# Optimization experiments

Hardware: AMD Instinct MI355X
Metric: run time of the kernel (lower is better)

The kernel has to match this reference:

```python
import jax, jax.numpy as jnp
import numpy as np

N = 16384   # total nodes
E = 49152   # total edges (avg degree 3, molecular)
NG = 512    # graphs in batch
DIM = 64    # hidden dim
NF = 11     # node features
EF = 4      # edge features
HID = 128   # edge-MLP hidden
JUMPS = 3
S2S_STEPS = 3


def _gru_step(x, h, w_ih, w_hh, b_ih, b_hh):
    gi = x @ w_ih.T + b_ih
    gh = h @ w_hh.T + b_hh
    ir, iz, inn = jnp.split(gi, 3, axis=-1)
    hr, hz, hn = jnp.split(gh, 3, axis=-1)
    r = jax.nn.sigmoid(ir + hr)
    z = jax.nn.sigmoid(iz + hz)
    n = jnp.tanh(inn + r * hn)
    return (1.0 - z) * n + z * h


def _lstm_step(x, h, c, w_ih, w_hh, b_ih, b_hh):
    g = x @ w_ih.T + b_ih + h @ w_hh.T + b_hh
    i, f, gg, o = jnp.split(g, 4, axis=-1)
    c2 = jax.nn.sigmoid(f) * c + jax.nn.sigmoid(i) * jnp.tanh(gg)
    h2 = jax.nn.sigmoid(o) * jnp.tanh(c2)
    return h2, c2


def _segment_softmax(e, seg, num_segments):
    m = jax.ops.segment_max(e, seg, num_segments)
    ex = jnp.exp(e - m[seg])
    s = jax.ops.segment_sum(ex, seg, num_segments)
    return ex / s[seg]


def setup_inputs() -> dict:
    key = jax.random.key(0)
    ks = jax.random.split(key, 16)
    def rn(k, shape, s=0.05):
        return jax.random.normal(k, shape, jnp.float32) * s
    x = jax.random.normal(ks[0], (N, NF), jnp.float32)
    edge_attr = jax.random.uniform(ks[1], (E, EF), dtype=jnp.float32)
    edge_index = jax.random.randint(ks[2], (2, E), 0, N)
    batch = jnp.sort(jax.random.randint(ks[3], (N,), 0, NG))
    z = lambda n: jnp.zeros((n,), jnp.float32)
    return {
        "x": x, "edge_attr": edge_attr, "edge_index": edge_index, "batch": batch,
        "lin0_w": rn(ks[4], (DIM, NF)), "lin0_b": z(DIM),
        "mlp_w1": rn(ks[5], (HID, EF)), "mlp_b1": z(HID),
        "mlp_w2": rn(ks[6], (DIM * DIM, HID)), "mlp_b2": z(DIM * DIM),
        "conv_root": rn(ks[7], (DIM, DIM)), "conv_bias": z(DIM),
        "gru_w_ih": rn(ks[8], (3 * DIM, DIM)), "gru_w_hh": rn(ks[9], (3 * DIM, DIM)),
        "gru_b_ih": z(3 * DIM), "gru_b_hh": z(3 * DIM),
        "lstm_w_ih": rn(ks[10], (4 * DIM, 2 * DIM)), "lstm_w_hh": rn(ks[11], (4 * DIM, DIM)),
        "lstm_b_ih": z(4 * DIM), "lstm_b_hh": z(4 * DIM),
        "lin1_w": rn(ks[12], (DIM, 2 * DIM)), "lin1_b": z(DIM),
        "lin2_w": rn(ks[13], (1, DIM)), "lin2_b": z(1),
    }


def reference(x, edge_attr, edge_index, batch,
              lin0_w, lin0_b, mlp_w1, mlp_b1, mlp_w2, mlp_b2,
              conv_root, conv_bias,
              gru_w_ih, gru_w_hh, gru_b_ih, gru_b_hh,
              lstm_w_ih, lstm_w_hh, lstm_b_ih, lstm_b_hh,
              lin1_w, lin1_b, lin2_w, lin2_b):
    src, dst = edge_index[0], edge_index[1]
    out = jax.nn.relu(x @ lin0_w.T + lin0_b)           # [N, DIM]
    h = out
    # edge-conditioned weights: MLP(edge_attr) -> [E, DIM, DIM]
    ew = (jax.nn.relu(edge_attr @ mlp_w1.T + mlp_b1) @ mlp_w2.T + mlp_b2)
    ew = ew.reshape(E, DIM, DIM)
    deg = jnp.maximum(jax.ops.segment_sum(jnp.ones((E,), out.dtype), dst, N), 1.0)
    for _ in range(JUMPS):
        msg = jnp.einsum('ei,eio->eo', out[src], ew)    # gather + per-edge matvec
        agg = jax.ops.segment_sum(msg, dst, N) / deg[:, None]  # mean aggr
        m = jax.nn.relu(agg + out @ conv_root + conv_bias)
        h = _gru_step(m, h, gru_w_ih, gru_w_hh, gru_b_ih, gru_b_hh)
        out = h
    # Set2Set pooling
    qh = jnp.zeros((NG, DIM), out.dtype)
    qc = jnp.zeros((NG, DIM), out.dtype)
    q_star = jnp.zeros((NG, 2 * DIM), out.dtype)
    for _ in range(S2S_STEPS):
        qh, qc = _lstm_step(q_star, qh, qc, lstm_w_ih, lstm_w_hh, lstm_b_ih, lstm_b_hh)
        e = jnp.sum(out * qh[batch], axis=-1)           # [N]
        a = _segment_softmax(e, batch, NG)
        r = jax.ops.segment_sum(a[:, None] * out, batch, NG)  # [NG, DIM]
        q_star = jnp.concatenate([qh, r], axis=-1)
    o = jax.nn.relu(q_star @ lin1_w.T + lin1_b)
    return (o @ lin2_w.T + lin2_b).reshape(-1)
```

## Files before the change

kernel.cpp:

```cpp
#include <hip/hip_runtime.h>
#include <hip/hip_bf16.h>

#define NN 16384
#define NE 49152
#define NGR 512
#define DIM 64
#define NF 11
#define EF 4
#define HID 128
#define JUMPS 3
#define S2S 3
#define TE 192
#define SUP 49152

typedef _Float16 v8h __attribute__((ext_vector_type(8)));
typedef _Float16 v4h __attribute__((ext_vector_type(4)));
typedef float v4f __attribute__((ext_vector_type(4)));

__device__ __forceinline__ float sigmoidf_(float x) { return 1.0f / (1.0f + __expf(-x)); }

__device__ __forceinline__ void async16(const void* g, void* l) {
  __builtin_amdgcn_global_load_lds(
      (const __attribute__((address_space(1))) unsigned int*)g,
      (__attribute__((address_space(3))) unsigned int*)l, 16, 0, 0);
}

#define B0 (NN / 256)
#define B1 (B0 + 112)
#define B2 (B1 + 192)
#define B3 (B2 + NN * DIM / 256)
#define B4 (B3 + 64 * 8192 / 256)
#define B5 (B4 + NE * HID / 256)
__global__ __launch_bounds__(256) void k_setup(const float* __restrict__ x,
                                               const float* __restrict__ l0w,
                                               const float* __restrict__ l0b,
                                               const float* __restrict__ ea,
                                               const float* __restrict__ w1,
                                               const float* __restrict__ b1,
                                               const float* __restrict__ w2,
                                               const float* __restrict__ conv_root,
                                               const float* __restrict__ gwih,
                                               const float* __restrict__ gwhh,
                                               const float* __restrict__ lwih,
                                               const float* __restrict__ lwhh,
                                               float* __restrict__ out, float* __restrict__ h,
                                               _Float16* __restrict__ hid,
                                               _Float16* __restrict__ Tgo,
                                               _Float16* __restrict__ pCr,
                                               _Float16* __restrict__ pW,
                                               float* __restrict__ W2,
                                               int* __restrict__ cnti) {
  int b = blockIdx.x, tid = threadIdx.x;
  if (b < B0) { cnti[b * 256 + tid] = 0; return; }
  if (b < B1) {
    int q = (b - B0) * 256 + tid;
    if (q < 4096) {
      int g = q >> 9, l = (q >> 3) & 63, j = q & 7;
      int ks = g >> 2, nt = g & 3;
      int k = ks * 32 + (l >> 4) * 8 + j, n = nt * 16 + (l & 15);
      pCr[q] = (_Float16)conv_root[k * 64 + n];
    } else if (q < 16384) {
      int q2 = q - 4096;
      int g = q2 >> 9, l = (q2 >> 3) & 63, j = q2 & 7;
      int ks = g / 12, nt = g % 12;
      int k = ks * 32 + (l >> 4) * 8 + j, n = nt * 16 + (l & 15);
      pW[q2] = (_Float16)gwih[n * 64 + k];
    } else {
      int q2 = q - 16384;
      int g = q2 >> 9, l = (q2 >> 3) & 63, j = q2 & 7;
      int ks = g / 12, nt = g % 12;
      int k = ks * 32 + (l >> 4) * 8 + j, n = nt * 16 + (l & 15);
      pW[12288 + q2] = (_Float16)gwhh[n * 64 + k];
    }
    return;
  }
  if (b < B2) {
    int i = (b - B1) * 256 + tid;
    int o = i / 192, k = i % 192;
    W2[i] = (k < 128) ? lwih[o * 128 + k] : lwhh[o * 64 + (k - 128)];
    return;
  }
  if (b < B3) {
    int idx = (b - B2) * 256 + tid;
    int n = idx >> 6, d = idx & 63;
    float acc = l0b[d];
#pragma unroll
    for (int f = 0; f < NF; ++f) acc += x[n * NF + f] * l0w[d * NF + f];
    acc = fmaxf(acc, 0.0f);
    out[idx] = acc; h[idx] = acc;
    return;
  }
  if (b < B4) {
    int idx = (b - B3) * 256 + tid;
    float v = w2[idx];
    int row = idx >> 7, hh = idx & 127;
    int i = row >> 6, n = row & 63;
    int nt = n >> 4, col = n & 15;
    int ks = hh >> 5, quad = (hh >> 3) & 3, j = hh & 7;
    int t = i * 16 + ks * 4 + nt;
    Tgo[(size_t)t * 512 + (quad * 16 + col) * 8 + j] = (_Float16)v;
    return;
  }
  {
    int idx = (b - B4) * 256 + tid;
    int e = idx >> 7, hh = idx & 127;
    float acc = b1[hh];
#pragma unroll
    for (int f = 0; f < EF; ++f) acc += ea[e * EF + f] * w1[hh * EF + f];
    hid[idx] = (_Float16)fmaxf(acc, 0.0f);
  }
}

__global__ __launch_bounds__(256) void k_count(const int* __restrict__ dst,
                                               int* __restrict__ cnti) {
  int e = blockIdx.x * 256 + threadIdx.x;
  atomicAdd(&cnti[dst[e]], 1);
}

__global__ __launch_bounds__(1024) void k_scan(const int* __restrict__ cnti,
                                               int* __restrict__ off) {
  __shared__ int wsum[16];
  int tid = threadIdx.x;
  int lane = tid & 63, wv = tid >> 6;
  int loc[16]; int sum = 0;
#pragma unroll
  for (int i = 0; i < 16; ++i) { loc[i] = sum; sum += cnti[tid * 16 + i]; }
  int inc = sum;
#pragma unroll
  for (int ofs = 1; ofs < 64; ofs <<= 1) {
    int t = __shfl_up(inc, ofs);
    if (lane >= ofs) inc += t;
  }
  if (lane == 63) wsum[wv] = inc;
  __syncthreads();
  if (wv == 0) {
    int w = (lane < 16) ? wsum[lane] : 0;
    int winc = w;
#pragma unroll
    for (int ofs = 1; ofs < 16; ofs <<= 1) {
      int t = __shfl_up(winc, ofs);
      if (lane >= ofs) winc += t;
    }
    if (lane < 16) wsum[lane] = winc - w;
  }
  __syncthreads();
  int base = wsum[wv] + (inc - sum);
#pragma unroll
  for (int i = 0; i < 16; ++i) off[tid * 16 + i] = base + loc[i];
  if (tid == 1023) off[NN] = base + sum;
}

__global__ __launch_bounds__(256) void k_scatter(const int* __restrict__ dst,
                                                 const int* __restrict__ off,
                                                 int* __restrict__ cnti,
                                                 int* __restrict__ epos) {
  int e = blockIdx.x * 256 + threadIdx.x;
  int d = dst[e];
  int s = atomicAdd(&cnti[d], -1);
  epos[e] = off[d] + s - 1;
}

__global__ __launch_bounds__(768, 3) void k_conv(const float* __restrict__ out,
                                                 const _Float16* __restrict__ hid,
                                                 const _Float16* __restrict__ Tgo,
                                                 const int* __restrict__ src,
                                                 const int* __restrict__ epos,
                                                 float* __restrict__ msg) {
  __shared__ char sRing[2 * SUP];
  __shared__ _Float16 sT[64 * TE];
  __shared__ int sE[TE];
  int tid = threadIdx.x;
  int wv = tid >> 6, lane = tid & 63;
  int kh = wv & 1, nh = (wv >> 1) & 1, mh = wv >> 2;
  int col = lane & 15, quad = lane >> 4;
  int e0 = blockIdx.x * TE;
  int phase = blockIdx.x % 21;

  if (tid < TE) sE[tid] = epos[e0 + tid];
  {
    int row = tid >> 2, seg = tid & 3;
    int loc = row & 63;
    int base = (row & ~63) + (loc & 15) * 4 + (loc >> 4);
    const float* srow = out + (size_t)src[e0 + row] * DIM + seg * 16;
#pragma unroll
    for (int f = 0; f < 16; ++f)
      sT[(seg * 16 + f) * TE + base] = (_Float16)srow[f];
  }

  v8h hf[4][2];
#pragma unroll
  for (int ms = 0; ms < 4; ++ms) {
    const _Float16* hrow = hid + (size_t)(e0 + mh * 64 + ms * 16 + col) * HID + kh * 64 + quad * 8;
#pragma unroll
    for (int k2 = 0; k2 < 2; ++k2) hf[ms][k2] = *(const v8h*)(hrow + k2 * 32);
  }

  __syncthreads();
  asm volatile("s_waitcnt vmcnt(0)" ::: "memory");

  const char* TgoB = (const char*)Tgo;
#pragma unroll
  for (int p = 0; p < 2; ++p) {
    int op = phase + p; if (op >= 21) op -= 21;
    const char* gp = TgoB + (size_t)op * SUP + wv * 4096 + lane * 16;
    char* lp = sRing + p * SUP + wv * 4096;
#pragma unroll
    for (int j = 0; j < 4; ++j) async16(gp + j * 1024, lp + j * 1024);
  }

  v4f acc[4][2];
#pragma unroll
  for (int ms = 0; ms < 4; ++ms)
#pragma unroll
    for (int nt = 0; nt < 2; ++nt) acc[ms][nt] = (v4f)(0.0f);

  for (int t = 0; t < 21; ++t) {
    int ot = phase + t; if (ot >= 21) ot -= 21;
    if (t < 20) asm volatile("s_waitcnt vmcnt(4)" ::: "memory");
    else        asm volatile("s_waitcnt vmcnt(0)" ::: "memory");
    asm volatile("s_barrier" ::: "memory");
    const char* sbase = sRing + (t & 1) * SUP;
#pragma unroll
    for (int cc = 0; cc < 3; ++cc) {
      int sp = ot * 3 + cc;
      const char* rb = sbase + cc * 16384;
      v8h bfr[2][2];
#pragma unroll
      for (int k2 = 0; k2 < 2; ++k2)
#pragma unroll
        for (int nt = 0; nt < 2; ++nt)
          bfr[k2][nt] = *(const v8h*)(rb + (((kh * 2 + k2) * 4 + nh * 2 + nt) * 64 + lane) * 16);
      v4h s4 = *(const v4h*)&sT[sp * TE + mh * 64 + col * 4];
#pragma unroll
      for (int ms = 0; ms < 4; ++ms) {
        _Float16 sv = s4[ms];
        v8h s8 = {sv, sv, sv, sv, sv, sv, sv, sv};
#pragma unroll
        for (int k2 = 0; k2 < 2; ++k2) {
          v8h az = hf[ms][k2] * s8;
#pragma unroll
          for (int nt = 0; nt < 2; ++nt)
            acc[ms][nt] = __builtin_amdgcn_mfma_f32_16x16x32_f16(az, bfr[k2][nt], acc[ms][nt], 0, 0, 0);
        }
      }
    }
    asm volatile("s_waitcnt lgkmcnt(0)" ::: "memory");
    if (t + 2 < 21) {
      int o2 = phase + t + 2; if (o2 >= 21) o2 -= 21;
      const char* gp = TgoB + (size_t)o2 * SUP + wv * 4096 + lane * 16;
      char* lp = sRing + (t & 1) * SUP + wv * 4096;
#pragma unroll
      for (int j = 0; j < 4; ++j) async16(gp + j * 1024, lp + j * 1024);
    }
  }

  if (wv < 4) {
    const char* gp = TgoB + (size_t)63 * 16384 + wv * 4096 + lane * 16;
    char* lp = sRing + SUP + wv * 4096;
#pragma unroll
    for (int j = 0; j < 4; ++j) async16(gp + j * 1024, lp + j * 1024);
  }
  asm volatile("s_waitcnt vmcnt(0)" ::: "memory");
  asm volatile("s_barrier" ::: "memory");
  {
    const char* rb = sRing + SUP;
    v8h bfr[2][2];
#pragma unroll
    for (int k2 = 0; k2 < 2; ++k2)
#pragma unroll
      for (int nt = 0; nt < 2; ++nt)
        bfr[k2][nt] = *(const v8h*)(rb + (((kh * 2 + k2) * 4 + nh * 2 + nt) * 64 + lane) * 16);
    v4h s4 = *(const v4h*)&sT[63 * TE + mh * 64 + col * 4];
#pragma unroll
    for (int ms = 0; ms < 4; ++ms) {
      _Float16 sv = s4[ms];
      v8h s8 = {sv, sv, sv, sv, sv, sv, sv, sv};
#pragma unroll
      for (int k2 = 0; k2 < 2; ++k2) {
        v8h az = hf[ms][k2] * s8;
#pragma unroll
        for (int nt = 0; nt < 2; ++nt)
          acc[ms][nt] = __builtin_amdgcn_mfma_f32_16x16x32_f16(az, bfr[k2][nt], acc[ms][nt], 0, 0, 0);
      }
    }
  }

  __syncthreads();
  float* aggL = (float*)sRing;
  if (kh == 0) {
#pragma unroll
    for (int ms = 0; ms < 4; ++ms)
#pragma unroll
      for (int r = 0; r < 4; ++r) {
        int row = mh * 64 + ms * 16 + quad * 4 + r;
#pragma unroll
        for (int nt = 0; nt < 2; ++nt)
          aggL[row * 66 + (nh * 2 + nt) * 16 + col] = acc[ms][nt][r];
      }
  }
  __syncthreads();
  if (kh == 1) {
#pragma unroll
    for (int ms = 0; ms < 4; ++ms)
#pragma unroll
      for (int r = 0; r < 4; ++r) {
        int row = mh * 64 + ms * 16 + quad * 4 + r;
#pragma unroll
        for (int nt = 0; nt < 2; ++nt) {
          int a = row * 66 + (nh * 2 + nt) * 16 + col;
          aggL[a] += acc[ms][nt][r];
        }
      }
  }
  __syncthreads();
  for (int idx = tid; idx < TE * 64; idx += 768) {
    int row = idx >> 6, c = idx & 63;
    msg[(size_t)sE[row] * DIM + c] = aggL[row * 66 + c];
  }
}

__global__ __launch_bounds__(256) void k_gru(const float* __restrict__ msg,
                                             const int* __restrict__ off,
                                             const _Float16* __restrict__ pCr,
                                             const _Float16* __restrict__ pW,
                                             const float* __restrict__ conv_bias,
                                             const float* __restrict__ bih,
                                             const float* __restrict__ bhh,
                                             float* __restrict__ out, float* __restrict__ h) {
  __shared__ _Float16 sW[24576];
  __shared__ _Float16 sMf[64][72];
  int tid = threadIdx.x;
  int w = tid >> 6, lane = tid & 63, col = lane & 15, quad = lane >> 4;
  int n0 = blockIdx.x * 64;
  int mrow = n0 + w * 16 + col;

  int go0[4], go1[4];
#pragma unroll
  for (int r = 0; r < 4; ++r) {
    int nd0 = n0 + w * 16 + quad * 4 + r;
    go0[r] = off[nd0]; go1[r] = off[nd0 + 1];
  }

  {
    int off2 = w * 12288 + lane * 16;
#pragma unroll
    for (int j = 0; j < 12; ++j)
      async16((const char*)pW + off2 + j * 1024, (char*)sW + off2 + j * 1024);
  }

  v8h afO[2], afH[2];
#pragma unroll
  for (int ks = 0; ks < 2; ++ks) {
    const float* p = out + (size_t)mrow * DIM + ks * 32 + quad * 8;
    float4 a = *(const float4*)p, b = *(const float4*)(p + 4);
    afO[ks] = (v8h){(_Float16)a.x, (_Float16)a.y, (_Float16)a.z, (_Float16)a.w,
                    (_Float16)b.x, (_Float16)b.y, (_Float16)b.z, (_Float16)b.w};
    const float* q = h + (size_t)mrow * DIM + ks * 32 + quad * 8;
    float4 c = *(const float4*)q, d = *(const float4*)(q + 4);
    afH[ks] = (v8h){(_Float16)c.x, (_Float16)c.y, (_Float16)c.z, (_Float16)c.w,
                    (_Float16)d.x, (_Float16)d.y, (_Float16)d.z, (_Float16)d.w};
  }

  v4f accC[4];
#pragma unroll
  for (int nt = 0; nt < 4; ++nt) accC[nt] = (v4f)(0.0f);
#pragma unroll
  for (int ks = 0; ks < 2; ++ks)
#pragma unroll
    for (int nt = 0; nt < 4; ++nt) {
      v8h bf = *(const v8h*)(pCr + (ks * 4 + nt) * 512 + lane * 8);
      accC[nt] = __builtin_amdgcn_mfma_f32_16x16x32_f16(afO[ks], bf, accC[nt], 0, 0, 0);
    }

#pragma unroll
  for (int r = 0; r < 4; ++r) {
    int nd = n0 + w * 16 + quad * 4 + r;
    int o0 = go0[r], o1 = go1[r];
    float dg = fmaxf((float)(o1 - o0), 1.0f);
    float s0 = 0.f, s1 = 0.f, s2 = 0.f, s3 = 0.f;
    for (int j = o0; j < o1; ++j) {
      const float* mr = msg + (size_t)j * DIM + col;
      s0 += mr[0]; s1 += mr[16]; s2 += mr[32]; s3 += mr[48];
    }
    float sv[4] = {s0, s1, s2, s3};
#pragma unroll
    for (int nt = 0; nt < 4; ++nt) {
      int o = nt * 16 + col;
      float mv = fmaxf(sv[nt] / dg + accC[nt][r] + conv_bias[o], 0.0f);
      sMf[nd - n0][o] = (_Float16)mv;
    }
  }
  __syncthreads();

  v8h afM[2];
#pragma unroll
  for (int ks = 0; ks < 2; ++ks)
    afM[ks] = *(const v8h*)&sMf[w * 16 + col][ks * 32 + quad * 8];

  v4f aRZ[8], aIN[4], aHN[4];
#pragma unroll
  for (int t = 0; t < 8; ++t) aRZ[t] = (v4f)(0.0f);
#pragma unroll
  for (int t = 0; t < 4; ++t) { aIN[t] = (v4f)(0.0f); aHN[t] = (v4f)(0.0f); }
#pragma unroll
  for (int ks = 0; ks < 2; ++ks) {
#pragma unroll
    for (int nt = 0; nt < 8; ++nt) {
      v8h bf1 = *(const v8h*)(sW + (ks * 12 + nt) * 512 + lane * 8);
      aRZ[nt] = __builtin_amdgcn_mfma_f32_16x16x32_f16(afM[ks], bf1, aRZ[nt], 0, 0, 0);
      v8h bf2 = *(const v8h*)(sW + 12288 + (ks * 12 + nt) * 512 + lane * 8);
      aRZ[nt] = __builtin_amdgcn_mfma_f32_16x16x32_f16(afH[ks], bf2, aRZ[nt], 0, 0, 0);
    }
#pragma unroll
    for (int nt = 8; nt < 12; ++nt) {
      v8h bf1 = *(const v8h*)(sW + (ks * 12 + nt) * 512 + lane * 8);
      aIN[nt - 8] = __builtin_amdgcn_mfma_f32_16x16x32_f16(afM[ks], bf1, aIN[nt - 8], 0, 0, 0);
      v8h bf2 = *(const v8h*)(sW + 12288 + (ks * 12 + nt) * 512 + lane * 8);
      aHN[nt - 8] = __builtin_amdgcn_mfma_f32_16x16x32_f16(afH[ks], bf2, aHN[nt - 8], 0, 0, 0);
    }
  }

#pragma unroll
  for (int r = 0; r < 4; ++r) {
    int nd = n0 + w * 16 + quad * 4 + r;
#pragma unroll
    for (int nt = 0; nt < 4; ++nt) {
      int d = nt * 16 + col;
      float rv = sigmoidf_(aRZ[nt][r] + bih[d] + bhh[d]);
      float zv = sigmoidf_(aRZ[nt + 4][r] + bih[64 + d] + bhh[64 + d]);
      float nv = tanhf(aIN[nt][r] + bih[128 + d] + rv * (aHN[nt][r] + bhh[128 + d]));
      float hold = h[(size_t)nd * DIM + d];
      float hn = (1.0f - zv) * nv + zv * hold;
      h[(size_t)nd * DIM + d] = hn;
      out[(size_t)nd * DIM + d] = hn;
    }
  }
}

__global__ __launch_bounds__(256) void k_s2s(const float* __restrict__ out,
                                             const int* __restrict__ batch,
                                             const float* __restrict__ W2,
                                             const float* __restrict__ lbih,
                                             const float* __restrict__ lbhh,
                                             const float* __restrict__ l1w,
                                             const float* __restrict__ l1b,
                                             const float* __restrict__ l2w,
                                             const float* __restrict__ l2b,
                                             float* __restrict__ outp) {
  __shared__ float sOut[128][64];
  __shared__ __align__(16) float sQ[192];
  __shared__ float sQc[64], sG[256], sR[4][64], sEv[256];
  __shared__ float sMv, sSum;
  __shared__ int sRange[2];
  int g = blockIdx.x, tid = threadIdx.x;
  int wv = tid >> 6, ln = tid & 63;

  if (tid < 2) {
    int target = g + tid;
    int lo = 0, hi = NN;
    while (lo < hi) { int mid = (lo + hi) >> 1; if (batch[mid] < target) lo = mid + 1; else hi = mid; }
    sRange[tid] = lo;
  }
  if (tid < 192) sQ[tid] = 0.0f;
  if (tid < 64) sQc[tid] = 0.0f;
  __syncthreads();
  int s0 = sRange[0], cnt = sRange[1] - sRange[0];
  int stg = cnt < 128 ? cnt : 128;
  for (int r = wv; r < stg; r += 4) sOut[r][ln] = out[(size_t)(s0 + r) * DIM + ln];
  __syncthreads();

  const float* wrow = W2 + (size_t)tid * 192;
  float bias = lbih[tid] + lbhh[tid];

  for (int step = 0; step < S2S; ++step) {
    v4f a4[8];
#pragma unroll
    for (int s = 0; s < 8; ++s) a4[s] = (v4f)(0.0f);
#pragma unroll
    for (int kb = 0; kb < 48; ++kb) {
      v4f w4 = *(const v4f*)(wrow + kb * 4);
      v4f q4 = *(const v4f*)&sQ[kb * 4];
      a4[kb & 7] += w4 * q4;
    }
    v4f t4 = a4[0] + a4[1] + a4[2] + a4[3] + a4[4] + a4[5] + a4[6] + a4[7];
    sG[tid] = bias + t4[0] + t4[1] + t4[2] + t4[3];
    __syncthreads();
    if (tid < 64) {
      float gi = sG[tid], gf = sG[64 + tid], gg = sG[128 + tid], go = sG[192 + tid];
      float c2 = sigmoidf_(gf) * sQc[tid] + sigmoidf_(gi) * tanhf(gg);
      sQc[tid] = c2;
      sQ[128 + tid] = sigmoidf_(go) * tanhf(c2);
    }
    __syncthreads();
    for (int r = wv; r < cnt; r += 4) {
      float v = (r < 128) ? sOut[r][ln] : out[(size_t)(s0 + r) * DIM + ln];
      float p = v * sQ[128 + ln];
#pragma unroll
      for (int off2 = 32; off2 >= 1; off2 >>= 1) p += __shfl_xor(p, off2);
      if (ln == 0 && r < 256) sEv[r] = p;
    }
    __syncthreads();
    if (wv == 0) {
      float mv = -1e30f;
      for (int r = ln; r < cnt; r += 64) mv = fmaxf(mv, sEv[r]);
#pragma unroll
      for (int off2 = 32; off2 >= 1; off2 >>= 1) mv = fmaxf(mv, __shfl_xor(mv, off2));
      float ss = 0.0f;
      for (int r = ln; r < cnt; r += 64) ss += __expf(sEv[r] - mv);
#pragma unroll
      for (int off2 = 32; off2 >= 1; off2 >>= 1) ss += __shfl_xor(ss, off2);
      if (ln == 0) { sMv = mv; sSum = ss; }
    }
    __syncthreads();
    float racc = 0.0f;
    for (int r = wv; r < cnt; r += 4) {
      float w = __expf(sEv[r] - sMv);
      float v = (r < 128) ? sOut[r][ln] : out[(size_t)(s0 + r) * DIM + ln];
      racc += w * v;
    }
    sR[wv][ln] = racc;
    __syncthreads();
    if (tid < 64) {
      float rv = sR[0][tid] + sR[1][tid] + sR[2][tid] + sR[3][tid];
      rv = (cnt > 0 && sSum > 0.0f) ? rv / sSum : 0.0f;
      sQ[tid] = sQ[128 + tid];
      sQ[64 + tid] = rv;
    }
    __syncthreads();
  }
  if (wv == 0) {
    const float* hrow = l1w + (size_t)ln * 128;
    v4f h4[4];
#pragma unroll
    for (int s = 0; s < 4; ++s) h4[s] = (v4f)(0.0f);
#pragma unroll
    for (int kb = 0; kb < 32; ++kb) {
      v4f w4 = *(const v4f*)(hrow + kb * 4);
      v4f q4 = *(const v4f*)&sQ[kb * 4];
      h4[kb & 3] += w4 * q4;
    }
    v4f u4 = h4[0] + h4[1] + h4[2] + h4[3];
    float acc = l1b[ln] + u4[0] + u4[1] + u4[2] + u4[3];
    acc = fmaxf(acc, 0.0f);
    float p = acc * l2w[ln];
#pragma unroll
    for (int off2 = 32; off2 >= 1; off2 >>= 1) p += __shfl_xor(p, off2);
    if (ln == 0) outp[g] = p + l2b[0];
  }
}

extern "C" void kernel_launch(void* const* d_in, const int* in_sizes, int n_in,
                              void* d_out, int out_size, void* d_ws, size_t ws_size,
                              hipStream_t stream) {
  const float* x         = (const float*)d_in[0];
  const float* ea        = (const float*)d_in[1];
  const int*   ei        = (const int*)d_in[2];
  const int*   batch     = (const int*)d_in[3];
  const float* lin0_w    = (const float*)d_in[4];
  const float* lin0_b    = (const float*)d_in[5];
  const float* w1        = (const float*)d_in[6];
  const float* b1        = (const float*)d_in[7];
  const float* w2        = (const float*)d_in[8];
  const float* conv_root = (const float*)d_in[10];
  const float* conv_bias = (const float*)d_in[11];
  const float* gwih      = (const float*)d_in[12];
  const float* gwhh      = (const float*)d_in[13];
  const float* gbih      = (const float*)d_in[14];
  const float* gbhh      = (const float*)d_in[15];
  const float* lwih      = (const float*)d_in[16];
  const float* lwhh      = (const float*)d_in[17];
  const float* lbih      = (const float*)d_in[18];
  const float* lbhh      = (const float*)d_in[19];
  const float* l1w       = (const float*)d_in[20];
  const float* l1b       = (const float*)d_in[21];
  const float* l2w       = (const float*)d_in[22];
  const float* l2b       = (const float*)d_in[23];
  float* outp = (float*)d_out;
  const int* srcI = ei;
  const int* dstI = ei + NE;

  char* ws = (char*)d_ws;
  size_t off0 = 0;
  auto alloc = [&](size_t bytes) -> char* {
    char* p = ws + off0;
    off0 = (off0 + bytes + 255) & ~(size_t)255;
    return p;
  };
  _Float16* hid  = (_Float16*)alloc((size_t)NE * HID * 2);
  _Float16* Tgo  = (_Float16*)alloc((size_t)64 * 8192 * 2);
  float* out_  = (float*)alloc((size_t)NN * DIM * 4);
  float* h     = (float*)alloc((size_t)NN * DIM * 4);
  float* msg   = (float*)alloc((size_t)NE * DIM * 4);
  int*   epos  = (int*)alloc((size_t)NE * 4);
  int*   off   = (int*)alloc(((size_t)NN + 1) * 4);
  int*   cnti  = (int*)alloc((size_t)NN * 4);
  _Float16* pCr  = (_Float16*)alloc(8 * 512 * 2);
  _Float16* pW   = (_Float16*)alloc(48 * 512 * 2);
  float* W2m   = (float*)alloc(256 * 192 * 4);
  (void)ws_size;

  dim3 B256(256), B768(768), B1024(1024);

  k_setup<<<B5, B256, 0, stream>>>(x, lin0_w, lin0_b, ea, w1, b1, w2, conv_root,
                                   gwih, gwhh, lwih, lwhh, out_, h, hid, Tgo,
                                   pCr, pW, W2m, cnti);
  k_count<<<NE / 256, B256, 0, stream>>>(dstI, cnti);
  k_scan<<<1, B1024, 0, stream>>>(cnti, off);
  k_scatter<<<NE / 256, B256, 0, stream>>>(dstI, off, cnti, epos);

  for (int jump = 0; jump < JUMPS; ++jump) {
    k_conv<<<NE / TE, B768, 0, stream>>>(out_, hid, Tgo, srcI, epos, msg);
    k_gru<<<NN / 64, B256, 0, stream>>>(msg, off, pCr, pW, conv_bias,
                                        gbih, gbhh, out_, h);
  }

  k_s2s<<<NGR, B256, 0, stream>>>(out_, batch, W2m, lbih, lbhh,
                                  l1w, l1b, l2w, l2b, outp);
}
```

Baseline: 352.4 us.

## Shrink GRU blocks to 16 nodes, split gate columns across waves, drop h

The GRU kernel now handles 16 nodes per 128-thread block instead of 64 nodes per 256-thread block. Each of the two waves computes half of the gate output columns, and the neighbour aggregation is split across the waves. The weights are no longer staged into shared memory; they are read straight from global memory, relying on cache. The separate h buffer is removed because it always equals out, which cuts one read and one write stream per node. The risks are redundant root-matmul work in both waves and uncached global weight reads, traded for four times as many blocks and lower LDS use.

```diff
diff --git a/kernel.cpp b/kernel.cpp
--- a/kernel.cpp
+++ b/kernel.cpp
@@ -43,7 +43,7 @@
                                                const float* __restrict__ gwhh,
                                                const float* __restrict__ lwih,
                                                const float* __restrict__ lwhh,
-                                               float* __restrict__ out, float* __restrict__ h,
+                                               float* __restrict__ out,
                                                _Float16* __restrict__ hid,
                                                _Float16* __restrict__ Tgo,
                                                _Float16* __restrict__ pCr,
@@ -86,8 +86,7 @@
     float acc = l0b[d];
 #pragma unroll
     for (int f = 0; f < NF; ++f) acc += x[n * NF + f] * l0w[d * NF + f];
-    acc = fmaxf(acc, 0.0f);
-    out[idx] = acc; h[idx] = acc;
+    out[idx] = fmaxf(acc, 0.0f);
     return;
   }
   if (b < B4) {
@@ -319,46 +318,34 @@
   }
 }
 
-__global__ __launch_bounds__(256) void k_gru(const float* __restrict__ msg,
+__global__ __launch_bounds__(128) void k_gru(const float* __restrict__ msg,
                                              const int* __restrict__ off,
                                              const _Float16* __restrict__ pCr,
                                              const _Float16* __restrict__ pW,
                                              const float* __restrict__ conv_bias,
                                              const float* __restrict__ bih,
                                              const float* __restrict__ bhh,
-                                             float* __restrict__ out, float* __restrict__ h) {
-  __shared__ _Float16 sW[24576];
-  __shared__ _Float16 sMf[64][72];
+                                             float* __restrict__ out) {
+  __shared__ __align__(16) _Float16 sMf[16][72];
   int tid = threadIdx.x;
-  int w = tid >> 6, lane = tid & 63, col = lane & 15, quad = lane >> 4;
-  int n0 = blockIdx.x * 64;
-  int mrow = n0 + w * 16 + col;
-
-  int go0[4], go1[4];
-#pragma unroll
-  for (int r = 0; r < 4; ++r) {
-    int nd0 = n0 + w * 16 + quad * 4 + r;
-    go0[r] = off[nd0]; go1[r] = off[nd0 + 1];
-  }
-
-  {
-    int off2 = w * 12288 + lane * 16;
-#pragma unroll
-    for (int j = 0; j < 12; ++j)
-      async16((const char*)pW + off2 + j * 1024, (char*)sW + off2 + j * 1024);
-  }
-
-  v8h afO[2], afH[2];
+  int wv2 = tid >> 6, lane = tid & 63, col = lane & 15, quad = lane >> 4;
+  int n0 = blockIdx.x * 16;
+
+  int go0[2], go1[2];
+#pragma unroll
+  for (int i = 0; i < 2; ++i) {
+    int nd0 = n0 + quad * 4 + wv2 * 2 + i;
+    go0[i] = off[nd0];
+    go1[i] = off[nd0 + 1];
+  }
+
+  v8h afO[2];
 #pragma unroll
   for (int ks = 0; ks < 2; ++ks) {
-    const float* p = out + (size_t)mrow * DIM + ks * 32 + quad * 8;
+    const float* p = out + (size_t)(n0 + col) * DIM + ks * 32 + quad * 8;
     float4 a = *(const float4*)p, b = *(const float4*)(p + 4);
     afO[ks] = (v8h){(_Float16)a.x, (_Float16)a.y, (_Float16)a.z, (_Float16)a.w,
                     (_Float16)b.x, (_Float16)b.y, (_Float16)b.z, (_Float16)b.w};
-    const float* q = h + (size_t)mrow * DIM + ks * 32 + quad * 8;
-    float4 c = *(const float4*)q, d = *(const float4*)(q + 4);
-    afH[ks] = (v8h){(_Float16)c.x, (_Float16)c.y, (_Float16)c.z, (_Float16)c.w,
-                    (_Float16)d.x, (_Float16)d.y, (_Float16)d.z, (_Float16)d.w};
   }
 
   v4f accC[4];
@@ -373,9 +360,10 @@
     }
 
 #pragma unroll
-  for (int r = 0; r < 4; ++r) {
-    int nd = n0 + w * 16 + quad * 4 + r;
-    int o0 = go0[r], o1 = go1[r];
+  for (int i = 0; i < 2; ++i) {
+    int r = wv2 * 2 + i;
+    int nd = n0 + quad * 4 + r;
+    int o0 = go0[i], o1 = go1[i];
     float dg = fmaxf((float)(o1 - o0), 1.0f);
     float s0 = 0.f, s1 = 0.f, s2 = 0.f, s3 = 0.f;
     for (int j = o0; j < o1; ++j) {
@@ -387,52 +375,53 @@
     for (int nt = 0; nt < 4; ++nt) {
       int o = nt * 16 + col;
       float mv = fmaxf(sv[nt] / dg + accC[nt][r] + conv_bias[o], 0.0f);
-      sMf[nd - n0][o] = (_Float16)mv;
-    }
+      sMf[quad * 4 + r][o] = (_Float16)mv;
+    }
+    (void)nd;
   }
   __syncthreads();
 
   v8h afM[2];
 #pragma unroll
   for (int ks = 0; ks < 2; ++ks)
-    afM[ks] = *(const v8h*)&sMf[w * 16 + col][ks * 32 + quad * 8];
-
-  v4f aRZ[8], aIN[4], aHN[4];
-#pragma unroll
-  for (int t = 0; t < 8; ++t) aRZ[t] = (v4f)(0.0f);
-#pragma unroll
-  for (int t = 0; t < 4; ++t) { aIN[t] = (v4f)(0.0f); aHN[t] = (v4f)(0.0f); }
-#pragma unroll
-  for (int ks = 0; ks < 2; ++ks) {
-#pragma unroll
-    for (int nt = 0; nt < 8; ++nt) {
-      v8h bf1 = *(const v8h*)(sW + (ks * 12 + nt) * 512 + lane * 8);
-      aRZ[nt] = __builtin_amdgcn_mfma_f32_16x16x32_f16(afM[ks], bf1, aRZ[nt], 0, 0, 0);
-      v8h bf2 = *(const v8h*)(sW + 12288 + (ks * 12 + nt) * 512 + lane * 8);
-      aRZ[nt] = __builtin_amdgcn_mfma_f32_16x16x32_f16(afH[ks], bf2, aRZ[nt], 0, 0, 0);
-    }
-#pragma unroll
-    for (int nt = 8; nt < 12; ++nt) {
-      v8h bf1 = *(const v8h*)(sW + (ks * 12 + nt) * 512 + lane * 8);
-      aIN[nt - 8] = __builtin_amdgcn_mfma_f32_16x16x32_f16(afM[ks], bf1, aIN[nt - 8], 0, 0, 0);
-      v8h bf2 = *(const v8h*)(sW + 12288 + (ks * 12 + nt) * 512 + lane * 8);
-      aHN[nt - 8] = __builtin_amdgcn_mfma_f32_16x16x32_f16(afH[ks], bf2, aHN[nt - 8], 0, 0, 0);
-    }
-  }
+    afM[ks] = *(const v8h*)&sMf[col][ks * 32 + quad * 8];
+
+  v4f aR[2], aZ[2], aIN[2], aHN[2];
+#pragma unroll
+  for (int t = 0; t < 2; ++t) {
+    aR[t] = (v4f)(0.0f); aZ[t] = (v4f)(0.0f);
+    aIN[t] = (v4f)(0.0f); aHN[t] = (v4f)(0.0f);
+  }
+#pragma unroll
+  for (int ks = 0; ks < 2; ++ks)
+#pragma unroll
+    for (int t = 0; t < 2; ++t) {
+      int tile = wv2 * 2 + t;
+      v8h bR1 = *(const v8h*)(pW + (ks * 12 + tile) * 512 + lane * 8);
+      aR[t] = __builtin_amdgcn_mfma_f32_16x16x32_f16(afM[ks], bR1, aR[t], 0, 0, 0);
+      v8h bR2 = *(const v8h*)(pW + 12288 + (ks * 12 + tile) * 512 + lane * 8);
+      aR[t] = __builtin_amdgcn_mfma_f32_16x16x32_f16(afO[ks], bR2, aR[t], 0, 0, 0);
+      v8h bZ1 = *(const v8h*)(pW + (ks * 12 + tile + 4) * 512 + lane * 8);
+      aZ[t] = __builtin_amdgcn_mfma_f32_16x16x32_f16(afM[ks], bZ1, aZ[t], 0, 0, 0);
+      v8h bZ2 = *(const v8h*)(pW + 12288 + (ks * 12 + tile + 4) * 512 + lane * 8);
+      aZ[t] = __builtin_amdgcn_mfma_f32_16x16x32_f16(afO[ks], bZ2, aZ[t], 0, 0, 0);
+      v8h bN1 = *(const v8h*)(pW + (ks * 12 + tile + 8) * 512 + lane * 8);
+      aIN[t] = __builtin_amdgcn_mfma_f32_16x16x32_f16(afM[ks], bN1, aIN[t], 0, 0, 0);
+      v8h bN2 = *(const v8h*)(pW + 12288 + (ks * 12 + tile + 8) * 512 + lane * 8);
+      aHN[t] = __builtin_amdgcn_mfma_f32_16x16x32_f16(afO[ks], bN2, aHN[t], 0, 0, 0);
+    }
 
 #pragma unroll
   for (int r = 0; r < 4; ++r) {
-    int nd = n0 + w * 16 + quad * 4 + r;
-#pragma unroll
-    for (int nt = 0; nt < 4; ++nt) {
-      int d = nt * 16 + col;
-      float rv = sigmoidf_(aRZ[nt][r] + bih[d] + bhh[d]);
-      float zv = sigmoidf_(aRZ[nt + 4][r] + bih[64 + d] + bhh[64 + d]);
-      float nv = tanhf(aIN[nt][r] + bih[128 + d] + rv * (aHN[nt][r] + bhh[128 + d]));
-      float hold = h[(size_t)nd * DIM + d];
-      float hn = (1.0f - zv) * nv + zv * hold;
-      h[(size_t)nd * DIM + d] = hn;
-      out[(size_t)nd * DIM + d] = hn;
+    int nd = n0 + quad * 4 + r;
+#pragma unroll
+    for (int t = 0; t < 2; ++t) {
+      int d = (wv2 * 2 + t) * 16 + col;
+      float rv = sigmoidf_(aR[t][r] + bih[d] + bhh[d]);
+      float zv = sigmoidf_(aZ[t][r] + bih[64 + d] + bhh[64 + d]);
+      float nv = tanhf(aIN[t][r] + bih[128 + d] + rv * (aHN[t][r] + bhh[128 + d]));
+      float hold = out[(size_t)nd * DIM + d];
+      out[(size_t)nd * DIM + d] = (1.0f - zv) * nv + zv * hold;
     }
   }
 }
@@ -589,7 +578,6 @@
   _Float16* hid  = (_Float16*)alloc((size_t)NE * HID * 2);
   _Float16* Tgo  = (_Float16*)alloc((size_t)64 * 8192 * 2);
   float* out_  = (float*)alloc((size_t)NN * DIM * 4);
-  float* h     = (float*)alloc((size_t)NN * DIM * 4);
   float* msg   = (float*)alloc((size_t)NE * DIM * 4);
   int*   epos  = (int*)alloc((size_t)NE * 4);
   int*   off   = (int*)alloc(((size_t)NN + 1) * 4);
@@ -599,10 +587,10 @@
   float* W2m   = (float*)alloc(256 * 192 * 4);
   (void)ws_size;
 
-  dim3 B256(256), B768(768), B1024(1024);
+  dim3 B128(128), B256(256), B768(768), B1024(1024);
 
   k_setup<<<B5, B256, 0, stream>>>(x, lin0_w, lin0_b, ea, w1, b1, w2, conv_root,
-                                   gwih, gwhh, lwih, lwhh, out_, h, hid, Tgo,
+                                   gwih, gwhh, lwih, lwhh, out_, hid, Tgo,
                                    pCr, pW, W2m, cnti);
   k_count<<<NE / 256, B256, 0, stream>>>(dstI, cnti);
   k_scan<<<1, B1024, 0, stream>>>(cnti, off);
@@ -610,8 +598,8 @@
 
   for (int jump = 0; jump < JUMPS; ++jump) {
     k_conv<<<NE / TE, B768, 0, stream>>>(out_, hid, Tgo, srcI, epos, msg);
-    k_gru<<<NN / 64, B256, 0, stream>>>(msg, off, pCr, pW, conv_bias,
-                                        gbih, gbhh, out_, h);
+    k_gru<<<NN / 16, B128, 0, stream>>>(msg, off, pCr, pW, conv_bias,
+                                        gbih, gbhh, out_);
   }
 
   k_s2s<<<NGR, B256, 0, stream>>>(out_, batch, W2m, lbih, lbhh,
```

After: 338.5 us. 1.04x faster.
